# Kernel optimization log

Hardware: AMD Instinct MI355X
Metric: run time of the kernel (lower is better)

Reference implementation:

```python
import jax, jax.numpy as jnp
import numpy as np

PS = 7          # window_size
HEADS = 8
DIM = 64
EPS = 1e-12     # F.normalize default eps


def resize_bilinear(x, oh, ow, align_corners):
    """PyTorch-style bilinear resize for NCHW tensors (antialias=False)."""
    b, c, h, w = x.shape
    if align_corners:
        ys = jnp.linspace(0.0, h - 1.0, oh, dtype=x.dtype)
        xs = jnp.linspace(0.0, w - 1.0, ow, dtype=x.dtype)
    else:
        ys = jnp.maximum((jnp.arange(oh, dtype=x.dtype) + 0.5) * (h / oh) - 0.5, 0.0)
        xs = jnp.maximum((jnp.arange(ow, dtype=x.dtype) + 0.5) * (w / ow) - 0.5, 0.0)
    y0 = jnp.floor(ys).astype(jnp.int32)
    x0 = jnp.floor(xs).astype(jnp.int32)
    y1 = jnp.minimum(y0 + 1, h - 1)
    x1 = jnp.minimum(x0 + 1, w - 1)
    ly = (ys - y0.astype(x.dtype))[None, None, :, None]   # (1,1,oh,1)
    lx = (xs - x0.astype(x.dtype))[None, None, None, :]   # (1,1,1,ow)
    rows = x[:, :, y0, :] * (1.0 - ly) + x[:, :, y1, :] * ly       # (b,c,oh,w)
    out = rows[:, :, :, x0] * (1.0 - lx) + rows[:, :, :, x1] * lx  # (b,c,oh,ow)
    return out


def _to_windows(t, b, heads, d, ps, xb, yb):
    # 'b (head d) (x h ph) (y w pw) -> (b x y) head d (w ph) (pw h)'
    t = t.reshape(b, heads, d, xb, ps, ps, yb, ps, ps)  # b,head,d,x,h,ph,y,w,pw
    t = t.transpose(0, 3, 6, 1, 2, 7, 5, 8, 4)          # b,x,y,head,d,w,ph,pw,h
    return t.reshape(b * xb * yb, heads, d, ps * ps, ps * ps)


def _from_windows(t, b, heads, d, ps, xb, yb):
    # inverse rearrange back to (b, head*d, x*ps*ps, y*ps*ps)
    t = t.reshape(b, xb, yb, heads, d, ps, ps, ps, ps)  # b,x,y,head,d,w,ph,pw,h
    t = t.transpose(0, 3, 4, 1, 8, 6, 2, 5, 7)          # b,head,d,x,h,ph,y,w,pw
    return t.reshape(b, heads * d, xb * ps * ps, yb * ps * ps)


def setup_inputs() -> dict:
    key = jax.random.key(0)
    k1, k2, k3, k4 = jax.random.split(key, 4)
    x = jax.random.normal(k1, (4, DIM, 256, 256), jnp.float32)
    qkv_w = jax.random.normal(k2, (3 * DIM, DIM), jnp.float32) * 0.05
    dw_w = jax.random.normal(k3, (3 * DIM, 1, 3, 3), jnp.float32) * 0.05
    proj_w = jax.random.normal(k4, (DIM, DIM), jnp.float32) * 0.05
    return {"x": x, "qkv_w": qkv_w, "dw_w": dw_w, "proj_w": proj_w}


def reference(x, qkv_w, dw_w, proj_w):
    b, c, h, w = x.shape
    heads, ps = HEADS, PS
    ps2 = ps * ps
    temph = -(-h // ps2) * ps2   # next multiple of ps^2 (matches while loop)
    tempw = -(-w // ps2) * ps2
    d = c // heads

    # conv1x1 (qkv) then depthwise 3x3 conv
    qkv = jnp.einsum('bchw,oc->bohw', x, qkv_w)
    qkv = jax.lax.conv_general_dilated(
        qkv, dw_w, window_strides=(1, 1), padding=((1, 1), (1, 1)),
        feature_group_count=3 * c,
        dimension_numbers=('NCHW', 'OIHW', 'NCHW'))

    # pad by bilinear interpolation, align_corners=True
    qkv = resize_bilinear(qkv, temph, tempw, align_corners=True)
    q, k, v = jnp.split(qkv, 3, axis=1)

    xb, yb = temph // ps2, tempw // ps2
    q = _to_windows(q, b, heads, d, ps, xb, yb)  # (b*xb*yb, heads, d, 49, 49)
    k = _to_windows(k, b, heads, d, ps, xb, yb)
    v = _to_windows(v, b, heads, d, ps, xb, yb)

    # L2-normalized (cosine) attention along the last axis, no temperature
    qn = q / jnp.maximum(jnp.linalg.norm(q, axis=-1, keepdims=True), EPS)
    kn = k / jnp.maximum(jnp.linalg.norm(k, axis=-1, keepdims=True), EPS)
    attn = jax.nn.softmax(qn @ jnp.swapaxes(kn, -1, -2), axis=-1)
    out = attn @ v

    out = _from_windows(out, b, heads, d, ps, xb, yb)
    out = resize_bilinear(out, h, w, align_corners=False)
    return jnp.einsum('bchw,oc->bohw', out, proj_w)
```

## Files before the change

kernel.cpp:

```cpp
#include <hip/hip_runtime.h>
#include <math.h>

#define BATCH 4
#define CIN 64
#define HW 256
#define NPIX 65536
#define OC 192
#define TH 294
#define NPIX_R 86436
#define PS2 49
#define C2N 2401
#define NWIN 36
#define WCPB 2304
#define KSTR 52
#define TABN (NWIN * C2N)

__device__ __forceinline__ float rl_f32(float v, int lane) {
    return __uint_as_float(__builtin_amdgcn_readlane(__float_as_uint(v), lane));
}

__global__ __launch_bounds__(256)
void k_qkv1x1(const float* __restrict__ x, const float* __restrict__ w,
              float* __restrict__ A) {
    __shared__ float wT[64][64];
    __shared__ float xs[64][256];
    x += (size_t)blockIdx.z * CIN * NPIX;
    A += (size_t)blockIdx.z * OC * NPIX;
    const int tid = threadIdx.x;
    const int pxbase = blockIdx.x * 256;
    const int ocbase = blockIdx.y * 64;

    for (int idx = tid; idx < 1024; idx += 256) {
        int o = idx >> 4, c4 = idx & 15;
        float4 v = *reinterpret_cast<const float4*>(w + (size_t)(ocbase + o) * CIN + c4 * 4);
        wT[c4 * 4 + 0][o] = v.x; wT[c4 * 4 + 1][o] = v.y;
        wT[c4 * 4 + 2][o] = v.z; wT[c4 * 4 + 3][o] = v.w;
    }
    for (int idx = tid; idx < 4096; idx += 256) {
        int c = idx >> 6, p4 = idx & 63;
        float4 v = *reinterpret_cast<const float4*>(x + (size_t)c * NPIX + pxbase + p4 * 4);
        *reinterpret_cast<float4*>(&xs[c][p4 * 4]) = v;
    }
    __syncthreads();

    const int tx = tid & 15, ty = tid >> 4;
    float acc[4][16];
    #pragma unroll
    for (int a = 0; a < 4; ++a)
        #pragma unroll
        for (int b = 0; b < 16; ++b) acc[a][b] = 0.f;

    #pragma unroll 4
    for (int k = 0; k < 64; ++k) {
        float4 wv = *reinterpret_cast<const float4*>(&wT[k][ty * 4]);
        float wr[4] = {wv.x, wv.y, wv.z, wv.w};
        float xv[16];
        #pragma unroll
        for (int i = 0; i < 4; ++i) {
            float4 v = *reinterpret_cast<const float4*>(&xs[k][tx * 4 + i * 64]);
            xv[i * 4 + 0] = v.x; xv[i * 4 + 1] = v.y;
            xv[i * 4 + 2] = v.z; xv[i * 4 + 3] = v.w;
        }
        #pragma unroll
        for (int a = 0; a < 4; ++a)
            #pragma unroll
            for (int b = 0; b < 16; ++b)
                acc[a][b] = fmaf(wr[a], xv[b], acc[a][b]);
    }

    #pragma unroll
    for (int a = 0; a < 4; ++a) {
        float* Ap = A + (size_t)(ocbase + ty * 4 + a) * NPIX + pxbase;
        #pragma unroll
        for (int i = 0; i < 4; ++i)
            *reinterpret_cast<float4*>(Ap + tx * 4 + i * 64) =
                make_float4(acc[a][i * 4 + 0], acc[a][i * 4 + 1],
                            acc[a][i * 4 + 2], acc[a][i * 4 + 3]);
    }
}

__global__ __launch_bounds__(256)
void k_dw3x3(const float* __restrict__ A, const float* __restrict__ dwv,
             float* __restrict__ Bf) {
    A  += (size_t)blockIdx.z * OC * NPIX;
    Bf += (size_t)blockIdx.z * OC * NPIX;
    int gid = blockIdx.x * 256 + threadIdx.x;
    int ch = gid >> 13;
    int q  = gid & 8191;
    int y  = q >> 5;
    int x8 = (q & 31) << 3;
    const float* Ap = A + (size_t)ch * NPIX;
    float wv[9];
    #pragma unroll
    for (int i = 0; i < 9; ++i) wv[i] = dwv[ch * 9 + i];
    float a[8];
    #pragma unroll
    for (int t = 0; t < 8; ++t) a[t] = 0.f;
    #pragma unroll
    for (int ky = 0; ky < 3; ++ky) {
        int yy = y + ky - 1;
        if (yy < 0 || yy >= HW) continue;
        const float* row = Ap + yy * HW;
        float4 m0 = *reinterpret_cast<const float4*>(row + x8);
        float4 m1 = *reinterpret_cast<const float4*>(row + x8 + 4);
        float lm = (x8 > 0)       ? row[x8 - 1] : 0.f;
        float rp = (x8 < HW - 8)  ? row[x8 + 8] : 0.f;
        float cv[10] = {lm, m0.x, m0.y, m0.z, m0.w, m1.x, m1.y, m1.z, m1.w, rp};
        #pragma unroll
        for (int kx = 0; kx < 3; ++kx) {
            float wk = wv[ky * 3 + kx];
            #pragma unroll
            for (int t = 0; t < 8; ++t)
                a[t] = fmaf(cv[t + kx], wk, a[t]);
        }
    }
    float* op = Bf + (size_t)ch * NPIX + y * HW + x8;
    *reinterpret_cast<float4*>(op)     = make_float4(a[0], a[1], a[2], a[3]);
    *reinterpret_cast<float4*>(op + 4) = make_float4(a[4], a[5], a[6], a[7]);
}

__global__ __launch_bounds__(256)
void k_prep(int4* __restrict__ itab, float4* __restrict__ wtab,
            int* __restrict__ dtab, int* __restrict__ otab) {
    const int w = blockIdx.x;
    const int xw = w / 6, yw = w - xw * 6;
    const float scale = 255.0f / 293.0f;
    for (int e = threadIdx.x; e < C2N; e += 256) {
        int rl = e / PS2, cl = e - rl * PS2;
        float sy = (float)(xw * PS2 + rl) * scale;
        float sx = (float)(yw * PS2 + cl) * scale;
        int y0 = (int)sy, x0 = (int)sx;
        float ly = sy - y0, lx = sx - x0;
        int y1 = min(y0 + 1, HW - 1), x1 = min(x0 + 1, HW - 1);
        itab[w * C2N + e] = make_int4(y0 * HW + x0, y0 * HW + x1,
                                      y1 * HW + x0, y1 * HW + x1);
        wtab[w * C2N + e] = make_float4((1.f - ly) * (1.f - lx), (1.f - ly) * lx,
                                        ly * (1.f - lx),         ly * lx);
        if (w == 0) {
            int i = (cl / 7) * 7 + rl % 7;
            int j = (cl % 7) * 7 + rl / 7;
            dtab[e] = i * KSTR + j;
            otab[e] = rl * TH + cl;
        }
    }
}

#define PIN4(v) asm volatile("" : "+v"(v.x), "+v"(v.y), "+v"(v.z), "+v"(v.w))
#define SQ4(v) fmaf(v.x, v.x, fmaf(v.y, v.y, fmaf(v.z, v.z, v.w * v.w)))
#define DOT4(KV, OFS) { float4 q_ = *reinterpret_cast<const float4*>(qr + (OFS)); \
    dd0 = fmaf(q_.x, KV.x, dd0); dd1 = fmaf(q_.y, KV.y, dd1); \
    dd2 = fmaf(q_.z, KV.z, dd2); dd3 = fmaf(q_.w, KV.w, dd3); }
#define PV4(VV, J) { \
    o0 = fmaf(rl_f32(p, (J)+0), VV.x, o0); o1 = fmaf(rl_f32(p, (J)+1), VV.y, o1); \
    o2 = fmaf(rl_f32(p, (J)+2), VV.z, o2); o3 = fmaf(rl_f32(p, (J)+3), VV.w, o3); }
#define VC(jj) (act ? Vs[(jj) * KSTR + l] : 1.0f)
#define GBODY(E) { \
    int4   o_  = itab[wbase + (E)]; \
    float4 wt_ = wtab[wbase + (E)]; \
    int    d_  = dtab[(E)]; \
    Qs[d_] = qb[o_.x] * wt_.x + qb[o_.y] * wt_.y + qb[o_.z] * wt_.z + qb[o_.w] * wt_.w; \
    Ks[d_] = kb[o_.x] * wt_.x + kb[o_.y] * wt_.y + kb[o_.z] * wt_.z + kb[o_.w] * wt_.w; \
    Vs[d_] = vb[o_.x] * wt_.x + vb[o_.y] * wt_.y + vb[o_.z] * wt_.z + vb[o_.w] * wt_.w; }

__global__ __launch_bounds__(256, 2)
void k_attn(const float* __restrict__ Bf,
            const int4* __restrict__ itab, const float4* __restrict__ wtab,
            const int* __restrict__ dtab, const int* __restrict__ otab,
            float* __restrict__ Cf) {
    __shared__ float Qs[PS2 * KSTR];
    __shared__ float Ks[PS2 * KSTR];
    __shared__ float Vs[PS2 * KSTR];
    Bf += (size_t)blockIdx.z * OC * NPIX;
    Cf += (size_t)blockIdx.z * (size_t)CIN * NPIX_R;
    const int tid = threadIdx.x;
    const int wv = tid >> 6, lane = tid & 63;
    const int wc  = blockIdx.x;
    const int ch  = wc & 63;
    const int win = wc >> 6;
    const int xw  = win / 6, yw = win - xw * 6;
    const float* qb = Bf + (size_t)ch * NPIX;
    const float* kb = qb + (size_t)64  * NPIX;
    const float* vb = qb + (size_t)128 * NPIX;
    const int wbase = win * C2N;

    #pragma unroll 3
    for (int it = 0; it < 9; ++it) {
        int e = tid + it * 256;
        GBODY(e)
    }
    if (tid < C2N - 2304) {
        GBODY(2304 + tid)
    }
    __syncthreads();

    const int l = min(lane, PS2 - 1);
    const bool act = (lane < PS2);

    const float* kr0 = &Ks[l * KSTR];
    float4 k0  = *reinterpret_cast<const float4*>(kr0 + 0);
    float4 k1  = *reinterpret_cast<const float4*>(kr0 + 4);
    float4 k2  = *reinterpret_cast<const float4*>(kr0 + 8);
    float4 k3  = *reinterpret_cast<const float4*>(kr0 + 12);
    float4 k4  = *reinterpret_cast<const float4*>(kr0 + 16);
    float4 k5  = *reinterpret_cast<const float4*>(kr0 + 20);
    float4 k6  = *reinterpret_cast<const float4*>(kr0 + 24);
    float4 k7  = *reinterpret_cast<const float4*>(kr0 + 28);
    float4 k8  = *reinterpret_cast<const float4*>(kr0 + 32);
    float4 k9  = *reinterpret_cast<const float4*>(kr0 + 36);
    float4 k10 = *reinterpret_cast<const float4*>(kr0 + 40);
    float4 k11 = *reinterpret_cast<const float4*>(kr0 + 44);
    float  k48 = kr0[48];
    PIN4(k0); PIN4(k1); PIN4(k2); PIN4(k3); PIN4(k4); PIN4(k5);
    PIN4(k6); PIN4(k7); PIN4(k8); PIN4(k9); PIN4(k10); PIN4(k11);

    float kss = SQ4(k0) + SQ4(k1) + SQ4(k2) + SQ4(k3) + SQ4(k4) + SQ4(k5)
              + SQ4(k6) + SQ4(k7) + SQ4(k8) + SQ4(k9) + SQ4(k10) + SQ4(k11)
              + k48 * k48;
    const float inkl = 1.f / fmaxf(sqrtf(kss), 1e-12f);

    float4 v0  = make_float4(VC(0),  VC(1),  VC(2),  VC(3));
    float4 v1  = make_float4(VC(4),  VC(5),  VC(6),  VC(7));
    float4 v2  = make_float4(VC(8),  VC(9),  VC(10), VC(11));
    float4 v3  = make_float4(VC(12), VC(13), VC(14), VC(15));
    float4 v4  = make_float4(VC(16), VC(17), VC(18), VC(19));
    float4 v5  = make_float4(VC(20), VC(21), VC(22), VC(23));
    float4 v6  = make_float4(VC(24), VC(25), VC(26), VC(27));
    float4 v7  = make_float4(VC(28), VC(29), VC(30), VC(31));
    float4 v8  = make_float4(VC(32), VC(33), VC(34), VC(35));
    float4 v9  = make_float4(VC(36), VC(37), VC(38), VC(39));
    float4 v10 = make_float4(VC(40), VC(41), VC(42), VC(43));
    float4 v11 = make_float4(VC(44), VC(45), VC(46), VC(47));
    float  v48 = VC(48);
    PIN4(v0); PIN4(v1); PIN4(v2); PIN4(v3); PIN4(v4); PIN4(v5);
    PIN4(v6); PIN4(v7); PIN4(v8); PIN4(v9); PIN4(v10); PIN4(v11);
    asm volatile("" : "+v"(k48), "+v"(v48));

    float inql;
    {
        const float* qrl = &Qs[l * KSTR];
        float qss = 0.f;
        #pragma unroll
        for (int u = 0; u < 12; ++u) {
            float4 t = *reinterpret_cast<const float4*>(qrl + u * 4);
            qss += SQ4(t);
        }
        float q48 = qrl[48];
        qss = fmaf(q48, q48, qss);
        inql = 1.f / fmaxf(sqrtf(qss), 1e-12f);
    }
    __syncthreads();

    for (int i = wv; i < PS2; i += 4) {
        const float inq_i = rl_f32(inql, i);
        const float* qr = &Qs[i * KSTR];
        float dd0 = 0.f, dd1 = 0.f, dd2 = 0.f, dd3 = 0.f;
        DOT4(k0, 0)   DOT4(k1, 4)   DOT4(k2, 8)   DOT4(k3, 12)
        DOT4(k4, 16)  DOT4(k5, 20)  DOT4(k6, 24)  DOT4(k7, 28)
        DOT4(k8, 32)  DOT4(k9, 36)  DOT4(k10, 40) DOT4(k11, 44)
        float dsum = (dd0 + dd1) + (dd2 + dd3);
        dsum = fmaf(qr[48], k48, dsum);
        float p = __expf(dsum * inkl * inq_i);

        float o0 = 0.f, o1 = 0.f, o2 = 0.f, o3 = 0.f;
        PV4(v0, 0)   PV4(v1, 4)   PV4(v2, 8)   PV4(v3, 12)
        PV4(v4, 16)  PV4(v5, 20)  PV4(v6, 24)  PV4(v7, 28)
        PV4(v8, 32)  PV4(v9, 36)  PV4(v10, 40) PV4(v11, 44)
        float ot = (o0 + o1) + (o2 + o3);
        ot = fmaf(rl_f32(p, 48), v48, ot);
        float ssum = rl_f32(ot, 49);
        float res = ot * __builtin_amdgcn_rcpf(ssum);
        if (act) Qs[i * KSTR + lane] = res;
    }
    __syncthreads();

    float* cb = Cf + (size_t)ch * NPIX_R + (xw * PS2) * TH + yw * PS2;
    for (int e = tid; e < C2N; e += 256)
        cb[otab[e]] = Qs[dtab[e]];
}

__global__ __launch_bounds__(256)
void k_downpmm(const float* __restrict__ Cf, const float* __restrict__ w,
               float* __restrict__ out) {
    __shared__ float wT[64][64];
    __shared__ float xs[64][256];
    Cf  += (size_t)blockIdx.z * (size_t)CIN * NPIX_R;
    out += (size_t)blockIdx.z * CIN * NPIX;
    const int tid = threadIdx.x;
    const int y = blockIdx.x;
    const float sc = 294.0f / 256.0f;
    float sy = fmaxf((y + 0.5f) * sc - 0.5f, 0.f);
    int y0 = (int)sy;
    float ly = sy - y0;
    int y1 = min(y0 + 1, TH - 1);
    float sx = fmaxf((tid + 0.5f) * sc - 0.5f, 0.f);
    int x0 = (int)sx;
    float lx = sx - x0;
    int x1 = min(x0 + 1, TH - 1);
    const float w00 = (1.f - ly) * (1.f - lx), w01 = (1.f - ly) * lx;
    const float w10 = ly * (1.f - lx),         w11 = ly * lx;

    for (int idx = tid; idx < 1024; idx += 256) {
        int o = idx >> 4, c4 = idx & 15;
        float4 v = *reinterpret_cast<const float4*>(w + (size_t)o * CIN + c4 * 4);
        wT[c4 * 4 + 0][o] = v.x; wT[c4 * 4 + 1][o] = v.y;
        wT[c4 * 4 + 2][o] = v.z; wT[c4 * 4 + 3][o] = v.w;
    }
    #pragma unroll 4
    for (int ch = 0; ch < 64; ++ch) {
        const float* r0 = Cf + (size_t)ch * NPIX_R + y0 * TH;
        const float* r1 = Cf + (size_t)ch * NPIX_R + y1 * TH;
        xs[ch][tid] = r0[x0] * w00 + r0[x1] * w01 + r1[x0] * w10 + r1[x1] * w11;
    }
    __syncthreads();

    const int tx = tid & 15, ty = tid >> 4;
    float acc[4][16];
    #pragma unroll
    for (int a = 0; a < 4; ++a)
        #pragma unroll
        for (int b = 0; b < 16; ++b) acc[a][b] = 0.f;

    #pragma unroll 4
    for (int k = 0; k < 64; ++k) {
        float4 wv = *reinterpret_cast<const float4*>(&wT[k][ty * 4]);
        float wr[4] = {wv.x, wv.y, wv.z, wv.w};
        float xv[16];
        #pragma unroll
        for (int i = 0; i < 4; ++i) {
            float4 v = *reinterpret_cast<const float4*>(&xs[k][tx * 4 + i * 64]);
            xv[i * 4 + 0] = v.x; xv[i * 4 + 1] = v.y;
            xv[i * 4 + 2] = v.z; xv[i * 4 + 3] = v.w;
        }
        #pragma unroll
        for (int a = 0; a < 4; ++a)
            #pragma unroll
            for (int b = 0; b < 16; ++b)
                acc[a][b] = fmaf(wr[a], xv[b], acc[a][b]);
    }

    #pragma unroll
    for (int a = 0; a < 4; ++a) {
        float* op = out + (size_t)(ty * 4 + a) * NPIX + y * HW;
        #pragma unroll
        for (int i = 0; i < 4; ++i)
            *reinterpret_cast<float4*>(op + tx * 4 + i * 64) =
                make_float4(acc[a][i * 4 + 0], acc[a][i * 4 + 1],
                            acc[a][i * 4 + 2], acc[a][i * 4 + 3]);
    }
}

extern "C" void kernel_launch(void* const* d_in, const int* in_sizes, int n_in,
                              void* d_out, int out_size, void* d_ws, size_t ws_size,
                              hipStream_t stream) {
    const float* x   = (const float*)d_in[0];
    const float* qw  = (const float*)d_in[1];
    const float* dwv = (const float*)d_in[2];
    const float* pw  = (const float*)d_in[3];
    float* out = (float*)d_out;

    const size_t perAB = (size_t)OC * NPIX;
    const size_t needBig = (size_t)2 * BATCH * perAB * sizeof(float);
    const size_t needMid = (size_t)2 * 2 * perAB * sizeof(float);

    int NB;
    if (ws_size >= needBig)      NB = BATCH;
    else if (ws_size >= needMid) NB = 2;
    else                         NB = 1;

    float* A = (float*)d_ws;
    float* B = A + (size_t)NB * perAB;
    float* C = A;
    float* T = A + (size_t)NB * CIN * NPIX_R;
    int4*   itab = (int4*)T;
    float4* wtab = (float4*)(T + (size_t)TABN * 4);
    int*    dtab = (int*)(T + (size_t)TABN * 8);
    int*    otab = dtab + C2N;

    for (int b = 0; b < BATCH; b += NB) {
        const float* xb = x + (size_t)b * CIN * NPIX;
        float* ob = out + (size_t)b * CIN * NPIX;
        hipLaunchKernelGGL(k_qkv1x1,  dim3(256, 3, NB),  dim3(256), 0, stream, xb, qw, A);
        hipLaunchKernelGGL(k_dw3x3,   dim3(6144, 1, NB), dim3(256), 0, stream, A, dwv, B);
        hipLaunchKernelGGL(k_prep,    dim3(NWIN, 1, 1),  dim3(256), 0, stream,
                           itab, wtab, dtab, otab);
        hipLaunchKernelGGL(k_attn,    dim3(WCPB, 1, NB), dim3(256), 0, stream,
                           B, itab, wtab, dtab, otab, C);
        hipLaunchKernelGGL(k_downpmm, dim3(256, 1, NB),  dim3(256), 0, stream, C, pw, ob);
    }
}
```

Before: 511.5 us.

## Fuse qkv 1x1 conv and depthwise 3x3 conv into one tiled kernel

Replaces the separate pointwise qkv GEMM and depthwise 3x3 kernels with a single kernel that loads a 18x18 halo tile of all 64 input channels into registers, computes each of the 192 output channels into shared memory, and immediately applies the 3x3 depthwise filter. This removes the global round trip of the 192-channel intermediate tensor. In exchange it recomputes halo pixels, serializes 192 channel iterations with a barrier each, reads weights directly from global memory, and runs only one block per tile with low occupancy.

```diff
diff --git a/kernel.cpp b/kernel.cpp
--- a/kernel.cpp
+++ b/kernel.cpp
@@ -19,104 +19,47 @@
     return __uint_as_float(__builtin_amdgcn_readlane(__float_as_uint(v), lane));
 }
 
-__global__ __launch_bounds__(256)
-void k_qkv1x1(const float* __restrict__ x, const float* __restrict__ w,
-              float* __restrict__ A) {
-    __shared__ float wT[64][64];
-    __shared__ float xs[64][256];
-    x += (size_t)blockIdx.z * CIN * NPIX;
-    A += (size_t)blockIdx.z * OC * NPIX;
+__global__ __launch_bounds__(384)
+void k_qkvdw(const float* __restrict__ x, const float* __restrict__ qw,
+             const float* __restrict__ dwv, float* __restrict__ Bf) {
+    __shared__ float qs[2][324];
+    x  += (size_t)blockIdx.z * CIN * NPIX;
+    Bf += (size_t)blockIdx.z * OC * NPIX;
     const int tid = threadIdx.x;
-    const int pxbase = blockIdx.x * 256;
-    const int ocbase = blockIdx.y * 64;
-
-    for (int idx = tid; idx < 1024; idx += 256) {
-        int o = idx >> 4, c4 = idx & 15;
-        float4 v = *reinterpret_cast<const float4*>(w + (size_t)(ocbase + o) * CIN + c4 * 4);
-        wT[c4 * 4 + 0][o] = v.x; wT[c4 * 4 + 1][o] = v.y;
-        wT[c4 * 4 + 2][o] = v.z; wT[c4 * 4 + 3][o] = v.w;
-    }
-    for (int idx = tid; idx < 4096; idx += 256) {
-        int c = idx >> 6, p4 = idx & 63;
-        float4 v = *reinterpret_cast<const float4*>(x + (size_t)c * NPIX + pxbase + p4 * 4);
-        *reinterpret_cast<float4*>(&xs[c][p4 * 4]) = v;
-    }
-    __syncthreads();
-
-    const int tx = tid & 15, ty = tid >> 4;
-    float acc[4][16];
+    const int ty = blockIdx.x >> 4, tx = blockIdx.x & 15;
+    const int oy = ty * 16, ox = tx * 16;
+
+    const int pr = tid / 18, pc = tid - pr * 18;
+    const int gy = oy - 1 + pr, gx = ox - 1 + pc;
+    const bool inb = (tid < 324) && (gy >= 0) && (gy < HW) &&
+                     (gx >= 0) && (gx < HW);
+    float xr[64];
+    const float* xp = x + gy * HW + gx;
     #pragma unroll
-    for (int a = 0; a < 4; ++a)
-        #pragma unroll
-        for (int b = 0; b < 16; ++b) acc[a][b] = 0.f;
-
-    #pragma unroll 4
-    for (int k = 0; k < 64; ++k) {
-        float4 wv = *reinterpret_cast<const float4*>(&wT[k][ty * 4]);
-        float wr[4] = {wv.x, wv.y, wv.z, wv.w};
-        float xv[16];
-        #pragma unroll
-        for (int i = 0; i < 4; ++i) {
-            float4 v = *reinterpret_cast<const float4*>(&xs[k][tx * 4 + i * 64]);
-            xv[i * 4 + 0] = v.x; xv[i * 4 + 1] = v.y;
-            xv[i * 4 + 2] = v.z; xv[i * 4 + 3] = v.w;
+    for (int c = 0; c < 64; ++c)
+        xr[c] = inb ? xp[(size_t)c * NPIX] : 0.f;
+
+    const int py = (tid & 255) >> 4, px = tid & 15;
+
+    for (int oc = 0; oc < OC; ++oc) {
+        const float* wr = qw + oc * CIN;
+        float acc = 0.f;
+        #pragma unroll
+        for (int c = 0; c < 64; ++c) acc = fmaf(xr[c], wr[c], acc);
+        if (tid < 324) qs[oc & 1][tid] = acc;
+        __syncthreads();
+        if (tid < 256) {
+            const float* q0 = qs[oc & 1];
+            const float* wd = dwv + oc * 9;
+            float s = 0.f;
+            #pragma unroll
+            for (int dy = 0; dy < 3; ++dy)
+                #pragma unroll
+                for (int dx = 0; dx < 3; ++dx)
+                    s = fmaf(q0[(py + dy) * 18 + (px + dx)], wd[dy * 3 + dx], s);
+            Bf[(size_t)oc * NPIX + (size_t)(oy + py) * HW + ox + px] = s;
         }
-        #pragma unroll
-        for (int a = 0; a < 4; ++a)
-            #pragma unroll
-            for (int b = 0; b < 16; ++b)
-                acc[a][b] = fmaf(wr[a], xv[b], acc[a][b]);
-    }
-
-    #pragma unroll
-    for (int a = 0; a < 4; ++a) {
-        float* Ap = A + (size_t)(ocbase + ty * 4 + a) * NPIX + pxbase;
-        #pragma unroll
-        for (int i = 0; i < 4; ++i)
-            *reinterpret_cast<float4*>(Ap + tx * 4 + i * 64) =
-                make_float4(acc[a][i * 4 + 0], acc[a][i * 4 + 1],
-                            acc[a][i * 4 + 2], acc[a][i * 4 + 3]);
-    }
-}
-
-__global__ __launch_bounds__(256)
-void k_dw3x3(const float* __restrict__ A, const float* __restrict__ dwv,
-             float* __restrict__ Bf) {
-    A  += (size_t)blockIdx.z * OC * NPIX;
-    Bf += (size_t)blockIdx.z * OC * NPIX;
-    int gid = blockIdx.x * 256 + threadIdx.x;
-    int ch = gid >> 13;
-    int q  = gid & 8191;
-    int y  = q >> 5;
-    int x8 = (q & 31) << 3;
-    const float* Ap = A + (size_t)ch * NPIX;
-    float wv[9];
-    #pragma unroll
-    for (int i = 0; i < 9; ++i) wv[i] = dwv[ch * 9 + i];
-    float a[8];
-    #pragma unroll
-    for (int t = 0; t < 8; ++t) a[t] = 0.f;
-    #pragma unroll
-    for (int ky = 0; ky < 3; ++ky) {
-        int yy = y + ky - 1;
-        if (yy < 0 || yy >= HW) continue;
-        const float* row = Ap + yy * HW;
-        float4 m0 = *reinterpret_cast<const float4*>(row + x8);
-        float4 m1 = *reinterpret_cast<const float4*>(row + x8 + 4);
-        float lm = (x8 > 0)       ? row[x8 - 1] : 0.f;
-        float rp = (x8 < HW - 8)  ? row[x8 + 8] : 0.f;
-        float cv[10] = {lm, m0.x, m0.y, m0.z, m0.w, m1.x, m1.y, m1.z, m1.w, rp};
-        #pragma unroll
-        for (int kx = 0; kx < 3; ++kx) {
-            float wk = wv[ky * 3 + kx];
-            #pragma unroll
-            for (int t = 0; t < 8; ++t)
-                a[t] = fmaf(cv[t + kx], wk, a[t]);
-        }
-    }
-    float* op = Bf + (size_t)ch * NPIX + y * HW + x8;
-    *reinterpret_cast<float4*>(op)     = make_float4(a[0], a[1], a[2], a[3]);
-    *reinterpret_cast<float4*>(op + 4) = make_float4(a[4], a[5], a[6], a[7]);
+    }
 }
 
 __global__ __launch_bounds__(256)
@@ -379,8 +322,8 @@
     for (int b = 0; b < BATCH; b += NB) {
         const float* xb = x + (size_t)b * CIN * NPIX;
         float* ob = out + (size_t)b * CIN * NPIX;
-        hipLaunchKernelGGL(k_qkv1x1,  dim3(256, 3, NB),  dim3(256), 0, stream, xb, qw, A);
-        hipLaunchKernelGGL(k_dw3x3,   dim3(6144, 1, NB), dim3(256), 0, stream, A, dwv, B);
+        hipLaunchKernelGGL(k_qkvdw,   dim3(256, 1, NB),  dim3(384), 0, stream,
+                           xb, qw, dwv, B);
         hipLaunchKernelGGL(k_prep,    dim3(NWIN, 1, 1),  dim3(256), 0, stream,
                            itab, wtab, dtab, otab);
         hipLaunchKernelGGL(k_attn,    dim3(WCPB, 1, NB), dim3(256), 0, stream,
```

Result: slower. 559.0 us (+9.3%).
